# Optimization experiments

Measured on AMD Instinct MI355X. Metric: run time of the kernel, lower is better.

Reference implementation:

```python
import jax, jax.numpy as jnp
import numpy as np

NEG_INF = -1e10
SLOPE = 0.01  # LeakyReLU default negative slope

def _lrelu(x):
    return jnp.where(x >= 0, x, SLOPE * x)

def setup_inputs() -> dict:
    key = jax.random.key(0)
    ks = jax.random.split(key, 12)
    B, L, D = 64, 512, 512
    s = 1.0 / np.sqrt(D)
    s2 = 1.0 / np.sqrt(2 * D)
    return {
        "r1": jax.random.normal(ks[0], (B, L, D), jnp.float32),
        "r2": jax.random.normal(ks[1], (B, L, D), jnp.float32),
        "mask1": jax.random.randint(ks[2], (B, L, 1), 0, 2, jnp.int32),
        "mask2": jax.random.randint(ks[3], (B, L, 1), 0, 2, jnp.int32),
        # mlp params (shared for r1 and r2, as in the torch module)
        "W1": jax.random.uniform(ks[4], (D, D), jnp.float32, -s, s),
        "b1": jnp.zeros((D,), jnp.float32),
        "W2": jax.random.uniform(ks[5], (D, D), jnp.float32, -s, s),
        "b2": jnp.zeros((D,), jnp.float32),
        # compare params
        "Wc1": jax.random.uniform(ks[6], (2 * D, D), jnp.float32, -s2, s2),
        "bc1": jnp.zeros((D,), jnp.float32),
        "Wc2": jax.random.uniform(ks[7], (D, D), jnp.float32, -s, s),
        "bc2": jnp.zeros((D,), jnp.float32),
    }

def reference(r1, r2, mask1, mask2, W1, b1, W2, b2, Wc1, bc1, Wc2, bc2):
    # dropout is inference-mode identity
    def mlp(x):
        return _lrelu(_lrelu(x @ W1 + b1) @ W2 + b2)

    def compare(x):
        return _lrelu(_lrelu(x @ Wc1 + bc1) @ Wc2 + bc2)

    m1 = mask1.astype(jnp.float32)  # [B,L1,1]
    m2 = mask2.astype(jnp.float32)  # [B,L2,1]
    r1m = mlp(r1) * m1
    r2m = mlp(r2) * m2

    # pairwise mask: >0 iff both tokens valid (magnitude from the D-dim matmul is irrelevant)
    mpos = m1 * jnp.swapaxes(m2, 1, 2)            # [B,L1,L2] in {0,1}
    mask_inf = jnp.where(mpos > 0, 0.0, NEG_INF)  # additive mask

    o = jnp.einsum('bik,bjk->bij', r1m, r2m) + mask_inf  # [B,L1,L2]
    o1 = jax.nn.softmax(o, axis=2) * mpos
    o2 = jax.nn.softmax(o, axis=1) * mpos

    r1_c = jnp.einsum('bij,bjd->bid', o1, r2m)  # [B,L1,D]
    r2_c = jnp.einsum('bij,bid->bjd', o2, r1m)  # [B,L2,D]

    r1_cmp = compare(jnp.concatenate([r1m, r1_c], axis=-1)) * m1
    r2_cmp = compare(jnp.concatenate([r2m, r2_c], axis=-1)) * m2
    return (r1_cmp, r2_cmp)
```

## Files before the change

kernel.cpp:

```cpp
#include <hip/hip_runtime.h>

#define LRELU_SLOPE 0.01f
#define NEG_BIG -1e10f

typedef unsigned short ushort_t;
typedef __bf16 bf16x8 __attribute__((ext_vector_type(8)));
typedef float f32x4 __attribute__((ext_vector_type(4)));

static __device__ __forceinline__ float lrelu_f(float x) {
    return x >= 0.0f ? x : LRELU_SLOPE * x;
}

static __device__ __forceinline__ ushort_t f2bf(float f) {
    unsigned int u = __float_as_uint(f);
    u += 0x7fffu + ((u >> 16) & 1u);
    return (ushort_t)(u >> 16);
}

static __device__ __forceinline__ void gld_lds16(const ushort_t* g, ushort_t* l) {
    __builtin_amdgcn_global_load_lds((const __attribute__((address_space(1))) void*)g,
                                     (__attribute__((address_space(3))) void*)l,
                                     16, 0, 0);
}

template<bool BIAS, bool LRELU, bool RM, bool PM, bool BF16OUT, bool TWOUT>
__global__ __launch_bounds__(1024, 4)
void gemm_nt(const ushort_t* __restrict__ A0, const ushort_t* __restrict__ A1,
             int Ksplit, int lda0, int lda1,
             const ushort_t* __restrict__ B, int ldb,
             const float* __restrict__ bias,
             const int* __restrict__ rm1, const int* __restrict__ rm2,
             void* __restrict__ C, int ldc,
             ushort_t* __restrict__ CT, int Mhalf,
             int M, int N, int K,
             long sA, long sB, long sC)
{
    __shared__ ushort_t lds[2][2][256 * 64];

    const unsigned nbx = gridDim.x, nby = gridDim.y;
    unsigned lin = blockIdx.x + nbx * (blockIdx.y + nby * blockIdx.z);
    const unsigned nwg = nbx * nby * gridDim.z;
    if ((nwg & 7u) == 0u)
        lin = (lin & 7u) * (nwg >> 3) + (lin >> 3);
    const unsigned bxs = lin % nbx;
    const unsigned t1  = lin / nbx;
    const unsigned bys = t1 % nby;
    const unsigned bzs = t1 / nby;

    const int bz   = (int)bzs;
    const int tid  = threadIdx.x;
    const int w    = tid >> 6;
    const int lane = tid & 63;
    const int wm   = w >> 2;
    const int wn   = w & 3;
    const int row0 = (int)bys * 256;
    const int col0 = (int)bxs * 256;

    const ushort_t* Ab0 = A0 + (long)bz * sA;
    const ushort_t* Ab1 = A1 + (long)bz * sA;
    const ushort_t* Bb  = B  + (long)bz * sB;

    const int srr = w * 16 + (lane >> 3);
    const int so  = (((lane & 7) ^ ((lane >> 3) & 7)) * 8);

    const int lr = lane & 15, q = lane >> 4;
    const int cx0 = ((q ^ (lr & 7)) * 8);
    const int cx1 = (((q + 4) ^ (lr & 7)) * 8);
    const int aRow = (wm * 64 + lr) * 64;
    const int bRow = (wn * 64 + lr) * 64;

    f32x4 acc[4][4] = {};

    auto stage = [&](int T, int buf) {
        const int k0g = T << 6;
        const ushort_t* Ap; int kk0, ldaP;
        if (k0g < Ksplit) { Ap = Ab0; kk0 = k0g;          ldaP = lda0; }
        else              { Ap = Ab1; kk0 = k0g - Ksplit; ldaP = lda1; }
        ushort_t* Ad = &lds[buf][0][0];
        ushort_t* Bd = &lds[buf][1][0];
        #pragma unroll
        for (int u = 0; u < 2; ++u)
            gld_lds16(Ap + (size_t)(row0 + srr + u * 8) * ldaP + kk0 + so,
                      Ad + (w * 16 + u * 8) * 64);
        #pragma unroll
        for (int u = 0; u < 2; ++u)
            gld_lds16(Bb + (size_t)(col0 + srr + u * 8) * ldb + k0g + so,
                      Bd + (w * 16 + u * 8) * 64);
    };

    const int NT = K >> 6;
    stage(0, 0);

    for (int T = 0; T < NT; ++T) {
        const int buf = T & 1;
        const ushort_t* Abuf = &lds[buf][0][0];
        const ushort_t* Bbuf = &lds[buf][1][0];

        __builtin_amdgcn_s_barrier();
        asm volatile("" ::: "memory");
        if (T + 1 < NT) {
            stage(T + 1, buf ^ 1);
            asm volatile("s_waitcnt vmcnt(4)" ::: "memory");
        } else {
            asm volatile("s_waitcnt vmcnt(0)" ::: "memory");
        }
        __builtin_amdgcn_s_barrier();
        asm volatile("" ::: "memory");

        #pragma unroll
        for (int kk = 0; kk < 2; ++kk) {
            const int cx = kk ? cx1 : cx0;
            bf16x8 af[4], bf[4];
            #pragma unroll
            for (int ii = 0; ii < 4; ++ii)
                af[ii] = *reinterpret_cast<const bf16x8*>(&Abuf[aRow + (ii * 16) * 64 + cx]);
            #pragma unroll
            for (int jj = 0; jj < 4; ++jj)
                bf[jj] = *reinterpret_cast<const bf16x8*>(&Bbuf[bRow + (jj * 16) * 64 + cx]);
            asm volatile("s_waitcnt lgkmcnt(0)" ::: "memory");
            __builtin_amdgcn_sched_barrier(0);
            __builtin_amdgcn_s_setprio(1);
            #pragma unroll
            for (int ii = 0; ii < 4; ++ii)
                #pragma unroll
                for (int jj = 0; jj < 4; ++jj)
                    acc[ii][jj] = __builtin_amdgcn_mfma_f32_16x16x32_bf16(
                        af[ii], bf[jj], acc[ii][jj], 0, 0, 0);
            __builtin_amdgcn_s_setprio(0);
        }
    }

    float biasv[4];
    int mj[4];
    #pragma unroll
    for (int j = 0; j < 4; ++j) {
        const int c = col0 + wn * 64 + j * 16 + lr;
        if (BIAS) biasv[j] = bias[c];
        if (PM)   mj[j] = rm2[(long)bz * N + c];
    }
    float* Cf = (float*)C + (long)bz * sC;
    ushort_t* Ch = (ushort_t*)C + (long)bz * sC;

    #pragma unroll
    for (int i = 0; i < 4; ++i) {
        const int rg0 = row0 + wm * 64 + i * 16 + q * 4;
        int mi4[4];
        if (RM || PM) {
            #pragma unroll
            for (int r = 0; r < 4; ++r) {
                const int row = rg0 + r;
                if (PM)      mi4[r] = rm1[(long)bz * M + row];
                else         mi4[r] = (row < Mhalf) ? rm1[row] : rm2[row - Mhalf];
            }
        }
        #pragma unroll
        for (int j = 0; j < 4; ++j) {
            const int c = col0 + wn * 64 + j * 16 + lr;
            ushort_t tp[4];
            #pragma unroll
            for (int r = 0; r < 4; ++r) {
                const int row = rg0 + r;
                float v = acc[i][j][r];
                if (BIAS) v += biasv[j];
                if (LRELU) v = lrelu_f(v);
                if (RM) v *= (float)mi4[r];
                if (PM) { if (!(mi4[r] && mj[j])) v += NEG_BIG; }
                const size_t a = (size_t)row * ldc + c;
                if (BF16OUT) Ch[a] = f2bf(v); else Cf[a] = v;
                if (TWOUT) tp[r] = f2bf(v);
            }
            if (TWOUT) {
                const size_t ta = ((size_t)(((rg0 >> 9) + 64) & 127)) * 262144
                                + (size_t)c * 512 + (rg0 & 511);
                *reinterpret_cast<uint2*>(CT + ta) = *reinterpret_cast<uint2*>(tp);
            }
        }
    }
}

__global__ __launch_bounds__(256)
void cvt2_f32_bf16(const float* __restrict__ a, const float* __restrict__ b,
                   ushort_t* __restrict__ oa, ushort_t* __restrict__ ob)
{
    const float* in = blockIdx.y ? b : a;
    ushort_t* out = blockIdx.y ? ob : oa;
    const long i = ((long)blockIdx.x * 256 + threadIdx.x) * 4;
    const float4 v = *reinterpret_cast<const float4*>(in + i);
    ushort_t o[4] = { f2bf(v.x), f2bf(v.y), f2bf(v.z), f2bf(v.w) };
    *reinterpret_cast<uint2*>(out + i) = *reinterpret_cast<uint2*>(o);
}

__global__ __launch_bounds__(256)
void transpose_cvt4(const float* __restrict__ W1, const float* __restrict__ W2,
                    const float* __restrict__ Wc1, const float* __restrict__ Wc2,
                    ushort_t* __restrict__ W1t, ushort_t* __restrict__ W2t,
                    ushort_t* __restrict__ Wc1t, ushort_t* __restrict__ Wc2t)
{
    __shared__ float t[32][33];
    const int z = blockIdx.z;
    const float* in = (z == 0) ? W1 : (z == 1) ? W2 : (z == 2) ? Wc1 : Wc2;
    ushort_t* out   = (z == 0) ? W1t : (z == 1) ? W2t : (z == 2) ? Wc1t : Wc2t;
    const int R = (z == 2) ? 1024 : 512;
    const int C = 512;
    const int c0 = blockIdx.x * 32, r0 = blockIdx.y * 32;
    if (r0 >= R) return;
    const int tx = threadIdx.x & 31, ty = threadIdx.x >> 5;
    #pragma unroll
    for (int p = 0; p < 4; ++p)
        t[ty + p * 8][tx] = in[(size_t)(r0 + ty + p * 8) * C + c0 + tx];
    __syncthreads();
    #pragma unroll
    for (int p = 0; p < 4; ++p)
        out[(size_t)(c0 + ty + p * 8) * R + r0 + tx] = f2bf(t[tx][ty + p * 8]);
}

__global__ __launch_bounds__(256)
void row_stats(const float* __restrict__ o, float* __restrict__ rmax,
               float* __restrict__ rsinv, int L)
{
    const int row  = blockIdx.x * 4 + (threadIdx.x >> 6);
    const int lane = threadIdx.x & 63;
    const float* p = o + (long)row * L;
    float m = -3.0e38f;
    for (int j = lane; j < L; j += 64) m = fmaxf(m, p[j]);
    #pragma unroll
    for (int off = 32; off > 0; off >>= 1) m = fmaxf(m, __shfl_xor(m, off));
    float s = 0.0f;
    for (int j = lane; j < L; j += 64) s += __expf(p[j] - m);
    #pragma unroll
    for (int off = 32; off > 0; off >>= 1) s += __shfl_xor(s, off);
    if (lane == 0) { rmax[row] = m; rsinv[row] = 1.0f / s; }
}

__global__ __launch_bounds__(256)
void col_part(const float* __restrict__ o, float* __restrict__ pm,
              float* __restrict__ ps, int L)
{
    const int b  = blockIdx.z;
    const int rc = blockIdx.y;
    const int j  = blockIdx.x * 256 + threadIdx.x;
    const float* p = o + (long)b * L * L + (long)rc * 64 * L + j;
    float m = -3.0e38f, s = 0.0f;
    #pragma unroll 4
    for (int i = 0; i < 64; ++i) {
        const float x = p[(long)i * L];
        const float mn = fmaxf(m, x);
        s = s * __expf(m - mn) + __expf(x - mn);
        m = mn;
    }
    const long idx = ((long)b * 8 + rc) * L + j;
    pm[idx] = m;
    ps[idx] = s;
}

__global__ __launch_bounds__(256)
void col_combine(const float* __restrict__ pm, const float* __restrict__ ps,
                 float* __restrict__ cmax, float* __restrict__ csinv, int L)
{
    const int b = blockIdx.y;
    const int j = blockIdx.x * 256 + threadIdx.x;
    float mk[8], sk[8];
    #pragma unroll
    for (int k = 0; k < 8; ++k) {
        mk[k] = pm[((long)b * 8 + k) * L + j];
        sk[k] = ps[((long)b * 8 + k) * L + j];
    }
    float m = -3.0e38f;
    #pragma unroll
    for (int k = 0; k < 8; ++k) m = fmaxf(m, mk[k]);
    float s = 0.0f;
    #pragma unroll
    for (int k = 0; k < 8; ++k) s += sk[k] * __expf(mk[k] - m);
    cmax[b * L + j]  = m;
    csinv[b * L + j] = 1.0f / s;
}

__global__ __launch_bounds__(256)
void softmax_apply(const float* __restrict__ o,
                   ushort_t* __restrict__ o1, ushort_t* __restrict__ o2T,
                   const float* __restrict__ rmax, const float* __restrict__ rsinv,
                   const float* __restrict__ cmax, const float* __restrict__ csinv,
                   const int* __restrict__ m1, const int* __restrict__ m2)
{
    __shared__ ushort_t t[32][33];
    const int b = blockIdx.z;
    const long bo = (long)b * 512 * 512;
    const int j0 = blockIdx.x * 32, i0 = blockIdx.y * 32;
    const int tx = threadIdx.x & 31, ty = threadIdx.x >> 5;
    const int col = b * 512 + j0 + tx;
    const int mjv = m2[col];
    const float cm = cmax[col], cs = csinv[col];
    #pragma unroll
    for (int p = 0; p < 4; ++p) {
        const int i = i0 + ty + p * 8;
        const int row = b * 512 + i;
        const float x = o[bo + (long)i * 512 + j0 + tx];
        const float mp = (m1[row] != 0 && mjv != 0) ? 1.0f : 0.0f;
        o1[bo + (long)i * 512 + j0 + tx] = f2bf(__expf(x - rmax[row]) * rsinv[row] * mp);
        t[ty + p * 8][tx] = f2bf(__expf(x - cm) * cs * mp);
    }
    __syncthreads();
    #pragma unroll
    for (int p = 0; p < 4; ++p)
        o2T[bo + (long)(j0 + ty + p * 8) * 512 + i0 + tx] = t[tx][ty + p * 8];
}

extern "C" void kernel_launch(void* const* d_in, const int* in_sizes, int n_in,
                              void* d_out, int out_size, void* d_ws, size_t ws_size,
                              hipStream_t stream)
{
    const float* r1  = (const float*)d_in[0];
    const float* r2  = (const float*)d_in[1];
    const int*   m1  = (const int*)d_in[2];
    const int*   m2  = (const int*)d_in[3];
    const float* W1  = (const float*)d_in[4];
    const float* b1v = (const float*)d_in[5];
    const float* W2  = (const float*)d_in[6];
    const float* b2v = (const float*)d_in[7];
    const float* Wc1 = (const float*)d_in[8];
    const float* bc1 = (const float*)d_in[9];
    const float* Wc2 = (const float*)d_in[10];
    const float* bc2 = (const float*)d_in[11];
    float* out = (float*)d_out;

    constexpr int  Bn = 64, L = 512, D = 512;
    constexpr long CE = (long)Bn * L * D;
    constexpr long S  = (long)L * L;
    constexpr int  NR = Bn * L;

    ushort_t* O    = (ushort_t*)d_out;
    ushort_t* r1b  = O;
    ushort_t* r2b  = O + CE;
    ushort_t* TT   = O;
    ushort_t* o1b  = O + 2 * CE;
    ushort_t* o2Tb = O + 3 * CE;

    char* wsb = (char*)d_ws;
    ushort_t* hb   = (ushort_t*)wsb;
    float*    obuf = (float*)wsb;
    ushort_t* r1c  = (ushort_t*)wsb;
    ushort_t* hc   = (ushort_t*)(wsb + 4 * CE);
    ushort_t* r1mb = (ushort_t*)(wsb + 8 * CE);
    ushort_t* r2mb = (ushort_t*)(wsb + 10 * CE);
    ushort_t* W1t  = (ushort_t*)(wsb + 12 * CE);
    ushort_t* W2t  = W1t + 512 * 512;
    ushort_t* Wc1t = W2t + 512 * 512;
    ushort_t* Wc2t = Wc1t + 512 * 1024;
    float* rmaxv = (float*)(Wc2t + 512 * 512);
    float* rsinv = rmaxv + NR;
    float* cmaxv = rsinv + NR;
    float* csinv = cmaxv + NR;
    float* pmbuf = csinv + NR;
    float* psbuf = pmbuf + 8 * L * Bn;

    const dim3 blk(256);
    const dim3 blkG(1024);
    const dim3 gD2(D / 256, 2 * NR / 256, 1);
    const dim3 gB(L / 256, L / 256, Bn);
    const dim3 gB2(L / 256, L / 256, 2 * Bn);

    cvt2_f32_bf16<<<dim3(CE / 1024, 2), blk, 0, stream>>>(r1, r2, r1b, r2b);
    transpose_cvt4<<<dim3(16, 32, 4), blk, 0, stream>>>(
        W1, W2, Wc1, Wc2, W1t, W2t, Wc1t, Wc2t);

    gemm_nt<true,true,false,false,true,false><<<gD2, blkG, 0, stream>>>(
        r1b, r1b, D, D, D, W1t, D, b1v, nullptr, nullptr, hb, D,
        nullptr, 0, 2 * NR, D, D, 0, 0, 0);
    gemm_nt<true,true,true,false,true,true><<<gD2, blkG, 0, stream>>>(
        hb, hb, D, D, D, W2t, D, b2v, m1, m2, r1mb, D,
        TT, NR, 2 * NR, D, D, 0, 0, 0);
    gemm_nt<false,false,false,true,false,false><<<gB, blkG, 0, stream>>>(
        r1mb, r1mb, D, D, D, r2mb, D, nullptr, m1, m2, obuf, L,
        nullptr, 0, L, L, D, S, S, S);
    row_stats<<<dim3(NR / 4), blk, 0, stream>>>(obuf, rmaxv, rsinv, L);
    col_part<<<dim3(L / 256, 8, Bn), blk, 0, stream>>>(obuf, pmbuf, psbuf, L);
    col_combine<<<dim3(L / 256, Bn), blk, 0, stream>>>(pmbuf, psbuf, cmaxv, csinv, L);
    softmax_apply<<<dim3(16, 16, Bn), blk, 0, stream>>>(
        obuf, o1b, o2Tb, rmaxv, rsinv, cmaxv, csinv, m1, m2);
    gemm_nt<false,false,false,false,true,false><<<gB2, blkG, 0, stream>>>(
        o1b, o1b, L, L, L, TT, L, nullptr, nullptr, nullptr, r1c, D,
        nullptr, 0, L, D, L, S, S, S);
    gemm_nt<true,true,false,false,true,false><<<gD2, blkG, 0, stream>>>(
        r1mb, r1c, D, D, D, Wc1t, 2 * D, bc1, nullptr, nullptr, hc, D,
        nullptr, 0, 2 * NR, D, 2 * D, 0, 0, 0);
    gemm_nt<true,true,true,false,false,false><<<gD2, blkG, 0, stream>>>(
        hc, hc, D, D, D, Wc2t, D, bc2, m1, m2, out, D,
        nullptr, NR, 2 * NR, D, D, 0, 0, 0);
}
```

Measured before the change: 609.4 us.

## Shrink GEMM tile to 256x128 with 512 threads and single-buffered LDS

Changes the bf16 MFMA GEMM from a 256x256 tile with 16 waves to a 256x128 tile with 8 waves, and grids double in the N dimension. The double-buffered LDS prefetch is removed: each K-step now loads and waits for its tile before computing. This cuts LDS use per block, which may let more blocks share a CU, but it gives up overlap of global loads with MFMA work and lowers reuse of the A tile.

```diff
diff --git a/kernel.cpp b/kernel.cpp
--- a/kernel.cpp
+++ b/kernel.cpp
@@ -24,7 +24,7 @@
 }
 
 template<bool BIAS, bool LRELU, bool RM, bool PM, bool BF16OUT, bool TWOUT>
-__global__ __launch_bounds__(1024, 4)
+__global__ __launch_bounds__(512, 4)
 void gemm_nt(const ushort_t* __restrict__ A0, const ushort_t* __restrict__ A1,
              int Ksplit, int lda0, int lda1,
              const ushort_t* __restrict__ B, int ldb,
@@ -35,7 +35,8 @@
              int M, int N, int K,
              long sA, long sB, long sC)
 {
-    __shared__ ushort_t lds[2][2][256 * 64];
+    __shared__ ushort_t As[256 * 64];
+    __shared__ ushort_t Bs[128 * 64];
 
     const unsigned nbx = gridDim.x, nby = gridDim.y;
     unsigned lin = blockIdx.x + nbx * (blockIdx.y + nby * blockIdx.z);
@@ -51,16 +52,17 @@
     const int tid  = threadIdx.x;
     const int w    = tid >> 6;
     const int lane = tid & 63;
-    const int wm   = w >> 2;
-    const int wn   = w & 3;
+    const int wm   = w >> 1;
+    const int wn   = w & 1;
     const int row0 = (int)bys * 256;
-    const int col0 = (int)bxs * 256;
+    const int col0 = (int)bxs * 128;
 
     const ushort_t* Ab0 = A0 + (long)bz * sA;
     const ushort_t* Ab1 = A1 + (long)bz * sA;
     const ushort_t* Bb  = B  + (long)bz * sB;
 
-    const int srr = w * 16 + (lane >> 3);
+    const int srA = w * 32 + (lane >> 3);
+    const int srB = w * 16 + (lane >> 3);
     const int so  = (((lane & 7) ^ ((lane >> 3) & 7)) * 8);
 
     const int lr = lane & 15, q = lane >> 4;
@@ -71,39 +73,28 @@
 
     f32x4 acc[4][4] = {};
 
-    auto stage = [&](int T, int buf) {
+    auto stage = [&](int T) {
         const int k0g = T << 6;
         const ushort_t* Ap; int kk0, ldaP;
         if (k0g < Ksplit) { Ap = Ab0; kk0 = k0g;          ldaP = lda0; }
         else              { Ap = Ab1; kk0 = k0g - Ksplit; ldaP = lda1; }
-        ushort_t* Ad = &lds[buf][0][0];
-        ushort_t* Bd = &lds[buf][1][0];
+        #pragma unroll
+        for (int u = 0; u < 4; ++u)
+            gld_lds16(Ap + (size_t)(row0 + srA + u * 8) * ldaP + kk0 + so,
+                      As + (w * 32 + u * 8) * 64);
         #pragma unroll
         for (int u = 0; u < 2; ++u)
-            gld_lds16(Ap + (size_t)(row0 + srr + u * 8) * ldaP + kk0 + so,
-                      Ad + (w * 16 + u * 8) * 64);
-        #pragma unroll
-        for (int u = 0; u < 2; ++u)
-            gld_lds16(Bb + (size_t)(col0 + srr + u * 8) * ldb + k0g + so,
-                      Bd + (w * 16 + u * 8) * 64);
+            gld_lds16(Bb + (size_t)(col0 + srB + u * 8) * ldb + k0g + so,
+                      Bs + (w * 16 + u * 8) * 64);
     };
 
     const int NT = K >> 6;
-    stage(0, 0);
 
     for (int T = 0; T < NT; ++T) {
-        const int buf = T & 1;
-        const ushort_t* Abuf = &lds[buf][0][0];
-        const ushort_t* Bbuf = &lds[buf][1][0];
-
         __builtin_amdgcn_s_barrier();
         asm volatile("" ::: "memory");
-        if (T + 1 < NT) {
-            stage(T + 1, buf ^ 1);
-            asm volatile("s_waitcnt vmcnt(4)" ::: "memory");
-        } else {
-            asm volatile("s_waitcnt vmcnt(0)" ::: "memory");
-        }
+        stage(T);
+        asm volatile("s_waitcnt vmcnt(0)" ::: "memory");
         __builtin_amdgcn_s_barrier();
         asm volatile("" ::: "memory");
 
@@ -113,10 +104,10 @@
             bf16x8 af[4], bf[4];
             #pragma unroll
             for (int ii = 0; ii < 4; ++ii)
-                af[ii] = *reinterpret_cast<const bf16x8*>(&Abuf[aRow + (ii * 16) * 64 + cx]);
+                af[ii] = *reinterpret_cast<const bf16x8*>(&As[aRow + (ii * 16) * 64 + cx]);
             #pragma unroll
             for (int jj = 0; jj < 4; ++jj)
-                bf[jj] = *reinterpret_cast<const bf16x8*>(&Bbuf[bRow + (jj * 16) * 64 + cx]);
+                bf[jj] = *reinterpret_cast<const bf16x8*>(&Bs[bRow + (jj * 16) * 64 + cx]);
             asm volatile("s_waitcnt lgkmcnt(0)" ::: "memory");
             __builtin_amdgcn_sched_barrier(0);
             __builtin_amdgcn_s_setprio(1);
@@ -354,10 +345,10 @@
     float* psbuf = pmbuf + 8 * L * Bn;
 
     const dim3 blk(256);
-    const dim3 blkG(1024);
-    const dim3 gD2(D / 256, 2 * NR / 256, 1);
-    const dim3 gB(L / 256, L / 256, Bn);
-    const dim3 gB2(L / 256, L / 256, 2 * Bn);
+    const dim3 blkG(512);
+    const dim3 gD2(D / 128, 2 * NR / 256, 1);
+    const dim3 gB(L / 128, L / 256, Bn);
+    const dim3 gB2(L / 128, L / 256, 2 * Bn);
 
     cvt2_f32_bf16<<<dim3(CE / 1024, 2), blk, 0, stream>>>(r1, r2, r1b, r2b);
     transpose_cvt4<<<dim3(16, 32, 4), blk, 0, stream>>>(
```

Measured after the change: 599.6 us. About the same (-1.6%).
